# Optimization experiments

Hardware: AMD Instinct MI355X
Metric: run time of the kernel (lower is better)

Reference implementation:

```python
import jax, jax.numpy as jnp
import numpy as np
from jax import lax

B, C, L = 8, 256, 2048
DK, DV, KS = 256, 256, 3
PAD = (KS - 1) // 2  # odd kernel -> dilation 1, same-length padding


def conv1d(x, w, b):
    # x: (B, C, L), w: (O, C, KS), b: (O,)
    y = lax.conv_general_dilated(
        x, w, window_strides=(1,), padding=[(PAD, PAD)],
        rhs_dilation=(1,), dimension_numbers=("NCH", "OIH", "NCH"))
    return y + b[None, :, None]


def setup_inputs() -> dict:
    key = jax.random.key(0)
    ks = jax.random.split(key, 7)
    sc = 1.0 / np.sqrt(C * KS)
    return {
        "x": jax.random.normal(ks[0], (B, C, L), dtype=jnp.float32),
        "Wq": jax.random.normal(ks[1], (DK, C, KS), dtype=jnp.float32) * sc,
        "bq": jnp.zeros((DK,), dtype=jnp.float32),
        "Wk": jax.random.normal(ks[2], (DK, C, KS), dtype=jnp.float32) * sc,
        "bk": jnp.zeros((DK,), dtype=jnp.float32),
        "Wv": jax.random.normal(ks[3], (DV, C, KS), dtype=jnp.float32) * sc,
        "bv": jnp.zeros((DV,), dtype=jnp.float32),
    }


def reference(x, Wq, bq, Wk, bk, Wv, bv):
    Q = conv1d(x, Wq, bq)  # (B, DK, L)
    K = conv1d(x, Wk, bk)  # (B, DK, L)
    V = conv1d(x, Wv, bv)  # (B, DV, L)
    # A = softmax(Q^T K / sqrt(dk)) over key axis
    scores = jnp.einsum("bdq,bdk->bqk", Q, K) / jnp.sqrt(jnp.float32(DK))
    A = jax.nn.softmax(scores, axis=2)  # (B, L, L)
    H = jnp.einsum("bqk,bdk->bdq", A, V)  # (B, DV, L)
    return H
```

## Files before the change

kernel.cpp:

```cpp
#include <hip/hip_runtime.h>
#include <hip/hip_bf16.h>
#include <stdint.h>


typedef __bf16 bf16;
typedef __bf16 bf16x2 __attribute__((ext_vector_type(2)));
typedef __bf16 bf16x4 __attribute__((ext_vector_type(4)));
typedef __bf16 bf16x8 __attribute__((ext_vector_type(8)));
typedef float f32x4 __attribute__((ext_vector_type(4)));
typedef uint32_t u32x4 __attribute__((ext_vector_type(4)));
typedef __attribute__((address_space(1))) const uint32_t cu32_as1;
typedef __attribute__((address_space(3))) uint32_t u32_as3;

#define DEVI __device__ __forceinline__
#define LOG2E 1.44269504088896f

DEVI void async_copy16(const void* g, void* l) {
  __builtin_amdgcn_global_load_lds((cu32_as1*)g, (u32_as3*)l, 16, 0, 0);
}

DEVI void block_sync() {
  asm volatile("" ::: "memory");
  __builtin_amdgcn_sched_barrier(0);
  __builtin_amdgcn_s_barrier();
  __builtin_amdgcn_sched_barrier(0);
  asm volatile("" ::: "memory");
}

#define VMCNT(n) asm volatile("s_waitcnt vmcnt(" #n ")" ::: "memory")

__global__ void prep_wx(const float* __restrict__ Wq, const float* __restrict__ Wk,
                        const float* __restrict__ Wv, const float* __restrict__ bq,
                        const float* __restrict__ bk, const float* __restrict__ bv,
                        bf16* __restrict__ W2, float* __restrict__ biasA,
                        const float* __restrict__ x, bf16* __restrict__ xT) {
  __shared__ float tile[64][33];
  const int blk = blockIdx.x;
  const int t = threadIdx.x;
  if (blk < 2304) {
    const float QSC = 0.0625f * LOG2E;
    int idx = blk * 256 + t;
    if (idx < 768 * 768) {
      int o = idx / 768, kk = idx - o * 768;
      int ks = kk >> 8, c = kk & 255;
      const float* W = (o < 256) ? Wq : ((o < 512) ? Wk : Wv);
      int ol = o & 255;
      float w = W[ol * 768 + c * 3 + ks];
      if (o < 256) w *= QSC;
      W2[o * 768 + kk] = (bf16)w;
    }
    if (idx < 768) {
      float v;
      if (idx < 256) v = bq[idx] * QSC;
      else if (idx < 512) v = bk[idx - 256];
      else v = bv[idx - 512];
      biasA[idx] = v;
    }
    return;
  }
  const int bid = blk - 2304;
  const int b = bid >> 8;
  const int rest = bid & 255;
  const int ct = rest & 3;
  const int lt = rest >> 2;
  const int c0 = ct * 64, l0 = lt * 32;
  const float* xb = x + (size_t)b * 256 * 2048;
#pragma unroll
  for (int i = 0; i < 8; ++i) {
    const int cc = (t >> 5) + i * 8;
    tile[cc][t & 31] = xb[(size_t)(c0 + cc) * 2048 + l0 + (t & 31)];
  }
  __syncthreads();
  bf16* xTb = xT + (size_t)b * 2050 * 256;
#pragma unroll
  for (int j = 0; j < 8; ++j) {
    const int ll = (t >> 6) + j * 4;
    xTb[(size_t)(l0 + ll + 1) * 256 + c0 + (t & 63)] = (bf16)tile[t & 63][ll];
  }
  if (lt == 0 && t < 64) xTb[c0 + t] = (bf16)0.f;
  if (lt == 63 && t < 64) xTb[(size_t)2049 * 256 + c0 + t] = (bf16)0.f;
}

__launch_bounds__(256, 2)
__global__ void conv_gemm(const bf16* __restrict__ W2, const bf16* __restrict__ xT,
                          const float* __restrict__ biasA, bf16* __restrict__ QT,
                          bf16* __restrict__ KT, bf16* __restrict__ V) {
  __shared__ bf16 Alds[128 * 64];
  __shared__ bf16 Blds[128 * 64];
  const int t = threadIdx.x;
  const int w = t >> 6, lane = t & 63;
  const int g = lane >> 4, lr = lane & 15;
  const int wr = w >> 1, wc = w & 1;
  const int bid = blockIdx.x;
  const int b = bid & 7;
  const int rest = bid >> 3;
  const int ot = rest % 6;
  const int lt = rest / 6;
  const int l0 = lt * 128;

  const bf16* xTb = xT + (size_t)b * 2050 * 256;
  const bf16* Ab = W2 + (size_t)(ot * 128) * 768;

  const int srow = t >> 3;
  const int scb = ((t & 7) * 16) ^ ((srow & 7) << 4);

  f32x4 acc[4][4];
#pragma unroll
  for (int i = 0; i < 4; ++i)
#pragma unroll
    for (int j = 0; j < 4; ++j) acc[i][j] = (f32x4){0.f, 0.f, 0.f, 0.f};

  for (int step = 0; step < 12; ++step) {
    const int kk = step * 64;
    const int ks = kk >> 8;
    const int c0 = kk & 255;
    const bf16* As = Ab + kk + (scb >> 1);
    const bf16* Bs = xTb + (size_t)(l0 + ks) * 256 + c0 + (scb >> 1);
#pragma unroll
    for (int i = 0; i < 4; ++i) {
      const int row = srow + i * 32;
      async_copy16(As + (size_t)row * 768, (char*)Alds + w * 1024 + i * 4096);
      async_copy16(Bs + (size_t)row * 256, (char*)Blds + w * 1024 + i * 4096);
    }
    asm volatile("s_waitcnt vmcnt(0)" ::: "memory");
    __syncthreads();
#pragma unroll
    for (int sub = 0; sub < 2; ++sub) {
      bf16x8 af[4], bfr[4];
#pragma unroll
      for (int mf = 0; mf < 4; ++mf) {
        const int row = wr * 64 + mf * 16 + lr;
        const int cb = (sub * 64 + g * 16) ^ ((row & 7) << 4);
        af[mf] = *(const bf16x8*)((const char*)Alds + row * 128 + cb);
      }
#pragma unroll
      for (int nf = 0; nf < 4; ++nf) {
        const int row = wc * 64 + nf * 16 + lr;
        const int cb = (sub * 64 + g * 16) ^ ((row & 7) << 4);
        bfr[nf] = *(const bf16x8*)((const char*)Blds + row * 128 + cb);
      }
#pragma unroll
      for (int mf = 0; mf < 4; ++mf)
#pragma unroll
        for (int nf = 0; nf < 4; ++nf)
          acc[mf][nf] = __builtin_amdgcn_mfma_f32_16x16x32_bf16(af[mf], bfr[nf], acc[mf][nf], 0, 0, 0);
    }
    __syncthreads();
  }

  const int obase = ot * 128 + wr * 64;
  const int lbase = l0 + wc * 64;
  if (ot < 4) {
    bf16* dst = ((ot < 2) ? QT : KT) + (size_t)b * 2048 * 256;
#pragma unroll
    for (int mf = 0; mf < 4; ++mf) {
      const int og = obase + mf * 16 + g * 4;
      float bb[4];
#pragma unroll
      for (int r = 0; r < 4; ++r) bb[r] = biasA[og + r];
#pragma unroll
      for (int nf = 0; nf < 4; ++nf) {
        const int l = lbase + nf * 16 + lr;
        bf16x4 pk;
#pragma unroll
        for (int r = 0; r < 4; ++r) pk[r] = (bf16)(acc[mf][nf][r] + bb[r]);
        *(bf16x4*)(dst + (size_t)l * 256 + (og & 255)) = pk;
      }
    }
  } else {
    bf16* dst = V + (size_t)b * 256 * 2048;
#pragma unroll
    for (int mf = 0; mf < 4; ++mf) {
      const int og = obase + mf * 16 + g * 4;
      float bb[4];
#pragma unroll
      for (int r = 0; r < 4; ++r) bb[r] = biasA[og + r];
      const int ov = og - 512;
#pragma unroll
      for (int nf = 0; nf < 4; ++nf) {
        const int l = lbase + nf * 16 + lr;
#pragma unroll
        for (int r = 0; r < 4; ++r)
          dst[(size_t)(ov + r) * 2048 + l] = (bf16)(acc[mf][nf][r] + bb[r]);
      }
    }
  }
}

__launch_bounds__(256, 2)
__global__ void attn(const bf16* __restrict__ QT, const bf16* __restrict__ KT,
                     const bf16* __restrict__ V, bf16* __restrict__ Opart,
                     float* __restrict__ Sl) {
  __shared__ bf16 Klds[2 * 32 * 256];
  __shared__ bf16 Vlds[128 * 64];
  const int t = threadIdx.x;
  const int w = t >> 6, lane = t & 63;
  const int g = lane >> 4, lr = lane & 15;
  const int bid = blockIdx.x;
  const int b = bid & 7;
  const int kvh = (bid >> 3) & 3;
  const int qt = bid >> 5;
  const int q0w = qt * 128 + w * 32;
  const int kb0 = kvh * 512;
  const bf16* QTb = QT + (size_t)b * 2048 * 256;
  const bf16* KTb = KT + (size_t)b * 2048 * 256;
  const bf16* Vb = V + (size_t)b * 256 * 2048;

  auto stageK = [&](int kt, int p) {
#pragma unroll
    for (int i = 0; i < 4; ++i) {
      const int row = i * 8 + (t >> 5);
      const int col = ((t & 31) ^ row) * 8;
      const bf16* src = KTb + (size_t)(kb0 + kt * 32 + row) * 256 + col;
      async_copy16(src, (char*)Klds + p * 16384 + i * 4096 + t * 16);
    }
  };
  auto stageV = [&](int kt) {
#pragma unroll
    for (int i = 0; i < 4; ++i) {
      const int row = i * 32 + (t >> 3);
      const int ls = (t & 7) ^ (row & 7);
      const int d = row * 2 + (ls >> 2);
      const int k0 = (ls & 3) * 8;
      const bf16* src = Vb + (size_t)d * 2048 + kb0 + kt * 32 + k0;
      async_copy16(src, (char*)Vlds + i * 4096 + t * 16);
    }
  };

  bf16x8 qreg[2][8];
#pragma unroll
  for (int qfr = 0; qfr < 2; ++qfr)
#pragma unroll
    for (int ds = 0; ds < 8; ++ds)
      qreg[qfr][ds] = *(const bf16x8*)(QTb + (size_t)(q0w + qfr * 16 + lr) * 256 + ds * 32 + g * 8);

  f32x4 oacc[16][2];
#pragma unroll
  for (int i = 0; i < 16; ++i) {
    oacc[i][0] = (f32x4){0.f, 0.f, 0.f, 0.f};
    oacc[i][1] = (f32x4){0.f, 0.f, 0.f, 0.f};
  }
  float l_acc[2] = {0.f, 0.f};

  stageV(0);
  stageK(0, 0);
  stageK(1, 1);

  for (int kt = 0; kt < 16; ++kt) {
    const int p = kt & 1;
    if (kt == 15) { VMCNT(0); } else { VMCNT(4); }
    block_sync();

    f32x4 sT[2][2];
#pragma unroll
    for (int kfr = 0; kfr < 2; ++kfr)
#pragma unroll
      for (int qfr = 0; qfr < 2; ++qfr) sT[kfr][qfr] = (f32x4){0.f, 0.f, 0.f, 0.f};
    __builtin_amdgcn_s_setprio(1);
#pragma unroll
    for (int ds = 0; ds < 8; ++ds) {
      bf16x8 kf[2];
#pragma unroll
      for (int kfr = 0; kfr < 2; ++kfr) {
        const int row = kfr * 16 + lr;
        kf[kfr] = *(const bf16x8*)((const char*)Klds + p * 16384 + row * 512 +
                                   (((ds * 4 + g) ^ row) * 16));
      }
#pragma unroll
      for (int kfr = 0; kfr < 2; ++kfr)
#pragma unroll
        for (int qfr = 0; qfr < 2; ++qfr)
          sT[kfr][qfr] = __builtin_amdgcn_mfma_f32_16x16x32_bf16(kf[kfr], qreg[qfr][ds], sT[kfr][qfr], 0, 0, 0);
    }
    __builtin_amdgcn_s_setprio(0);

#pragma unroll
    for (int kfr = 0; kfr < 2; ++kfr)
#pragma unroll
      for (int qfr = 0; qfr < 2; ++qfr)
#pragma unroll
        for (int r = 0; r < 4; ++r) {
          float pe = __builtin_exp2f(sT[kfr][qfr][r]);
          sT[kfr][qfr][r] = pe;
          l_acc[qfr] += pe;
        }

    bf16x8 pB[2];
#pragma unroll
    for (int qfr = 0; qfr < 2; ++qfr) {
      uint32_t wq[2][2];
#pragma unroll
      for (int kfr = 0; kfr < 2; ++kfr)
#pragma unroll
        for (int pp = 0; pp < 2; ++pp) {
          bf16x2 pr;
          pr[0] = (bf16)sT[kfr][qfr][2 * pp];
          pr[1] = (bf16)sT[kfr][qfr][2 * pp + 1];
          wq[kfr][pp] = __builtin_bit_cast(uint32_t, pr);
        }
      uint32_t bw[4];
#pragma unroll
      for (int j = 0; j < 4; ++j) {
        const int srcLane = ((g & 1) * 2 + (j >> 1)) * 16 + lr;
        const uint32_t a = (uint32_t)__shfl((int)wq[0][j & 1], srcLane, 64);
        const uint32_t bb = (uint32_t)__shfl((int)wq[1][j & 1], srcLane, 64);
        bw[j] = (lane < 32) ? a : bb;
      }
      u32x4 v4 = {bw[0], bw[1], bw[2], bw[3]};
      pB[qfr] = __builtin_bit_cast(bf16x8, v4);
    }

    __builtin_amdgcn_s_setprio(1);
#pragma unroll
    for (int dfr = 0; dfr < 16; ++dfr) {
      const int row = dfr * 8 + (lr >> 1);
      bf16x8 vf = *(const bf16x8*)((const char*)Vlds + row * 128 +
                                   ((((lr & 1) * 4 + g) ^ ((lr >> 1) & 7)) * 16));
      oacc[dfr][0] = __builtin_amdgcn_mfma_f32_16x16x32_bf16(vf, pB[0], oacc[dfr][0], 0, 0, 0);
      oacc[dfr][1] = __builtin_amdgcn_mfma_f32_16x16x32_bf16(vf, pB[1], oacc[dfr][1], 0, 0, 0);
    }
    __builtin_amdgcn_s_setprio(0);
    block_sync();
    if (kt < 15) stageV(kt + 1);
    if (kt < 14) stageK(kt + 2, p);
  }

#pragma unroll
  for (int qfr = 0; qfr < 2; ++qfr) {
    float rv = l_acc[qfr];
    rv += __shfl_xor(rv, 16, 64);
    rv += __shfl_xor(rv, 32, 64);
    l_acc[qfr] = rv;
  }

  bf16* Op = Opart + (size_t)bid * 128 * 256;
#pragma unroll
  for (int qfr = 0; qfr < 2; ++qfr) {
    const int ql = w * 32 + qfr * 16 + lr;
#pragma unroll
    for (int dfr = 0; dfr < 16; ++dfr) {
      const int d0 = dfr * 16 + g * 4;
      bf16x4 pk;
#pragma unroll
      for (int r = 0; r < 4; ++r) pk[r] = (bf16)oacc[dfr][qfr][r];
      *(bf16x4*)(Op + (size_t)ql * 256 + d0) = pk;
    }
    if (g == 0) Sl[bid * 128 + ql] = l_acc[qfr];
  }
}

__launch_bounds__(256)
__global__ void merge_p(const bf16* __restrict__ Opart, const float* __restrict__ Sl,
                        float* __restrict__ H) {
  __shared__ float Ocomb[32][257];
  const int bid = blockIdx.x;
  const int b = bid & 7;
  const int qt = (bid >> 3) & 15;
  const int qc = bid >> 7;
  const int t = threadIdx.x;
  const int g2 = t >> 5, lane2 = t & 31;
  float* Hb = H + (size_t)b * 256 * 2048 + qt * 128 + qc * 32;

#pragma unroll
  for (int qb = 0; qb < 4; ++qb) {
    const int qq = qb * 8 + g2;
    const int ql = qc * 32 + qq;
    float wsum = 0.f;
    float o[8];
#pragma unroll
    for (int j = 0; j < 8; ++j) o[j] = 0.f;
#pragma unroll
    for (int kvh = 0; kvh < 4; ++kvh) {
      const int blk = b + 8 * kvh + 32 * qt;
      wsum += Sl[blk * 128 + ql];
      bf16x8 v = *(const bf16x8*)(Opart + ((size_t)blk * 128 + ql) * 256 + lane2 * 8);
#pragma unroll
      for (int j = 0; j < 8; ++j) o[j] += (float)v[j];
    }
    const float inv = 1.f / wsum;
#pragma unroll
    for (int j = 0; j < 8; ++j) Ocomb[qq][lane2 * 8 + j] = o[j] * inv;
  }
  __syncthreads();
  const int q = t & 31;
  const int dbase = (t >> 5) * 32;
#pragma unroll
  for (int j = 0; j < 32; ++j) {
    const int d = dbase + j;
    Hb[(size_t)d * 2048 + q] = Ocomb[q][d];
  }
}

extern "C" void kernel_launch(void* const* d_in, const int* in_sizes, int n_in,
                              void* d_out, int out_size, void* d_ws, size_t ws_size,
                              hipStream_t stream) {
  (void)in_sizes; (void)n_in; (void)out_size; (void)ws_size;
  const float* x = (const float*)d_in[0];
  const float* Wq = (const float*)d_in[1];
  const float* bq = (const float*)d_in[2];
  const float* Wk = (const float*)d_in[3];
  const float* bk = (const float*)d_in[4];
  const float* Wv = (const float*)d_in[5];
  const float* bv = (const float*)d_in[6];
  char* ws = (char*)d_ws;
  bf16* xT = (bf16*)(ws + 0);
  bf16* W2 = (bf16*)(ws + 8396800);
  float* biasA = (float*)(ws + 9576448);
  bf16* QT = (bf16*)(ws + 9580544);
  bf16* KT = (bf16*)(ws + 17969152);
  bf16* V = (bf16*)(ws + 26357760);
  bf16* Opart = (bf16*)(ws + 34746368);
  float* Sl = (float*)(ws + 68300800);
  float* H = (float*)d_out;

  prep_wx<<<dim3(4352), dim3(256), 0, stream>>>(Wq, Wk, Wv, bq, bk, bv, W2, biasA, x, xT);
  conv_gemm<<<dim3(768), dim3(256), 0, stream>>>(W2, xT, biasA, QT, KT, V);
  attn<<<dim3(512), dim3(256), 0, stream>>>(QT, KT, V, Opart, Sl);
  merge_p<<<dim3(512), dim3(256), 0, stream>>>(Opart, Sl, H);
}
```

Before: 106.1 us.

## Use 64-key tiles with split K/V staging and 16x16x16 MFMA for PV

The attention kernel now processes 64 keys per iteration instead of 32 and drops the double-buffered K tile. K for the next tile is prefetched right after the QK^T MFMAs, and V after the PV MFMAs. The PV product switches to the 16x16x16 bf16 MFMA so the exponentiated scores can feed the B operand directly from the QK accumulator layout, removing the cross-lane shuffle repack. The trade-off is twice as many narrower MFMAs for PV, extra barriers per iteration, and K loads that are less overlapped without double buffering.

```diff
diff --git a/kernel.cpp b/kernel.cpp
--- a/kernel.cpp
+++ b/kernel.cpp
@@ -4,11 +4,10 @@
 
 
 typedef __bf16 bf16;
-typedef __bf16 bf16x2 __attribute__((ext_vector_type(2)));
 typedef __bf16 bf16x4 __attribute__((ext_vector_type(4)));
 typedef __bf16 bf16x8 __attribute__((ext_vector_type(8)));
+typedef short s16x4 __attribute__((ext_vector_type(4)));
 typedef float f32x4 __attribute__((ext_vector_type(4)));
-typedef uint32_t u32x4 __attribute__((ext_vector_type(4)));
 typedef __attribute__((address_space(1))) const uint32_t cu32_as1;
 typedef __attribute__((address_space(3))) uint32_t u32_as3;
 
@@ -191,8 +190,8 @@
 __global__ void attn(const bf16* __restrict__ QT, const bf16* __restrict__ KT,
                      const bf16* __restrict__ V, bf16* __restrict__ Opart,
                      float* __restrict__ Sl) {
-  __shared__ bf16 Klds[2 * 32 * 256];
-  __shared__ bf16 Vlds[128 * 64];
+  __shared__ bf16 Klds[64 * 256];
+  __shared__ bf16 Vlds[256 * 64];
   const int t = threadIdx.x;
   const int w = t >> 6, lane = t & 63;
   const int g = lane >> 4, lr = lane & 15;
@@ -206,23 +205,21 @@
   const bf16* KTb = KT + (size_t)b * 2048 * 256;
   const bf16* Vb = V + (size_t)b * 256 * 2048;
 
-  auto stageK = [&](int kt, int p) {
-#pragma unroll
-    for (int i = 0; i < 4; ++i) {
+  auto stageK = [&](int kt) {
+#pragma unroll
+    for (int i = 0; i < 8; ++i) {
       const int row = i * 8 + (t >> 5);
-      const int col = ((t & 31) ^ row) * 8;
-      const bf16* src = KTb + (size_t)(kb0 + kt * 32 + row) * 256 + col;
-      async_copy16(src, (char*)Klds + p * 16384 + i * 4096 + t * 16);
+      const int col = ((t & 31) ^ (row & 31)) * 8;
+      const bf16* src = KTb + (size_t)(kb0 + kt * 64 + row) * 256 + col;
+      async_copy16(src, (char*)Klds + i * 4096 + t * 16);
     }
   };
   auto stageV = [&](int kt) {
 #pragma unroll
-    for (int i = 0; i < 4; ++i) {
+    for (int i = 0; i < 8; ++i) {
       const int row = i * 32 + (t >> 3);
-      const int ls = (t & 7) ^ (row & 7);
-      const int d = row * 2 + (ls >> 2);
-      const int k0 = (ls & 3) * 8;
-      const bf16* src = Vb + (size_t)d * 2048 + kb0 + kt * 32 + k0;
+      const int koff = ((t & 7) ^ (row & 7)) * 8;
+      const bf16* src = Vb + (size_t)row * 2048 + kb0 + kt * 64 + koff;
       async_copy16(src, (char*)Vlds + i * 4096 + t * 16);
     }
   };
@@ -242,87 +239,71 @@
   }
   float l_acc[2] = {0.f, 0.f};
 
+  stageK(0);
   stageV(0);
-  stageK(0, 0);
-  stageK(1, 1);
-
-  for (int kt = 0; kt < 16; ++kt) {
-    const int p = kt & 1;
-    if (kt == 15) { VMCNT(0); } else { VMCNT(4); }
+
+  for (int kt = 0; kt < 8; ++kt) {
+    VMCNT(8);
     block_sync();
 
-    f32x4 sT[2][2];
-#pragma unroll
-    for (int kfr = 0; kfr < 2; ++kfr)
+    f32x4 sT[4][2];
+#pragma unroll
+    for (int kfr = 0; kfr < 4; ++kfr)
 #pragma unroll
       for (int qfr = 0; qfr < 2; ++qfr) sT[kfr][qfr] = (f32x4){0.f, 0.f, 0.f, 0.f};
     __builtin_amdgcn_s_setprio(1);
 #pragma unroll
     for (int ds = 0; ds < 8; ++ds) {
-      bf16x8 kf[2];
-#pragma unroll
-      for (int kfr = 0; kfr < 2; ++kfr) {
+      bf16x8 kf[4];
+#pragma unroll
+      for (int kfr = 0; kfr < 4; ++kfr) {
         const int row = kfr * 16 + lr;
-        kf[kfr] = *(const bf16x8*)((const char*)Klds + p * 16384 + row * 512 +
-                                   (((ds * 4 + g) ^ row) * 16));
-      }
-#pragma unroll
-      for (int kfr = 0; kfr < 2; ++kfr)
+        kf[kfr] = *(const bf16x8*)((const char*)Klds + row * 512 +
+                                   (((ds * 4 + g) ^ (row & 31)) * 16));
+      }
+#pragma unroll
+      for (int kfr = 0; kfr < 4; ++kfr)
 #pragma unroll
         for (int qfr = 0; qfr < 2; ++qfr)
           sT[kfr][qfr] = __builtin_amdgcn_mfma_f32_16x16x32_bf16(kf[kfr], qreg[qfr][ds], sT[kfr][qfr], 0, 0, 0);
     }
     __builtin_amdgcn_s_setprio(0);
-
-#pragma unroll
-    for (int kfr = 0; kfr < 2; ++kfr)
-#pragma unroll
-      for (int qfr = 0; qfr < 2; ++qfr)
+    block_sync();
+    if (kt < 7) stageK(kt + 1);
+
+    s16x4 pB16[4][2];
+#pragma unroll
+    for (int kfr = 0; kfr < 4; ++kfr)
+#pragma unroll
+      for (int qfr = 0; qfr < 2; ++qfr) {
+        bf16x4 pk;
 #pragma unroll
         for (int r = 0; r < 4; ++r) {
           float pe = __builtin_exp2f(sT[kfr][qfr][r]);
-          sT[kfr][qfr][r] = pe;
           l_acc[qfr] += pe;
+          pk[r] = (bf16)pe;
         }
-
-    bf16x8 pB[2];
-#pragma unroll
-    for (int qfr = 0; qfr < 2; ++qfr) {
-      uint32_t wq[2][2];
-#pragma unroll
-      for (int kfr = 0; kfr < 2; ++kfr)
-#pragma unroll
-        for (int pp = 0; pp < 2; ++pp) {
-          bf16x2 pr;
-          pr[0] = (bf16)sT[kfr][qfr][2 * pp];
-          pr[1] = (bf16)sT[kfr][qfr][2 * pp + 1];
-          wq[kfr][pp] = __builtin_bit_cast(uint32_t, pr);
-        }
-      uint32_t bw[4];
-#pragma unroll
-      for (int j = 0; j < 4; ++j) {
-        const int srcLane = ((g & 1) * 2 + (j >> 1)) * 16 + lr;
-        const uint32_t a = (uint32_t)__shfl((int)wq[0][j & 1], srcLane, 64);
-        const uint32_t bb = (uint32_t)__shfl((int)wq[1][j & 1], srcLane, 64);
-        bw[j] = (lane < 32) ? a : bb;
-      }
-      u32x4 v4 = {bw[0], bw[1], bw[2], bw[3]};
-      pB[qfr] = __builtin_bit_cast(bf16x8, v4);
-    }
+        pB16[kfr][qfr] = __builtin_bit_cast(s16x4, pk);
+      }
+
+    VMCNT(8);
+    block_sync();
 
     __builtin_amdgcn_s_setprio(1);
 #pragma unroll
     for (int dfr = 0; dfr < 16; ++dfr) {
-      const int row = dfr * 8 + (lr >> 1);
-      bf16x8 vf = *(const bf16x8*)((const char*)Vlds + row * 128 +
-                                   ((((lr & 1) * 4 + g) ^ ((lr >> 1) & 7)) * 16));
-      oacc[dfr][0] = __builtin_amdgcn_mfma_f32_16x16x32_bf16(vf, pB[0], oacc[dfr][0], 0, 0, 0);
-      oacc[dfr][1] = __builtin_amdgcn_mfma_f32_16x16x32_bf16(vf, pB[1], oacc[dfr][1], 0, 0, 0);
+      const int row = dfr * 16 + lr;
+#pragma unroll
+      for (int kfr = 0; kfr < 4; ++kfr) {
+        const int slot = (kfr * 2 + (g >> 1)) ^ (row & 7);
+        s16x4 vf = *(const s16x4*)((const char*)Vlds + row * 128 + slot * 16 + (g & 1) * 8);
+        oacc[dfr][0] = __builtin_amdgcn_mfma_f32_16x16x16bf16_1k(vf, pB16[kfr][0], oacc[dfr][0], 0, 0, 0);
+        oacc[dfr][1] = __builtin_amdgcn_mfma_f32_16x16x16bf16_1k(vf, pB16[kfr][1], oacc[dfr][1], 0, 0, 0);
+      }
     }
     __builtin_amdgcn_s_setprio(0);
     block_sync();
-    if (kt < 15) stageV(kt + 1);
-    if (kt < 14) stageK(kt + 2, p);
+    if (kt < 7) stageV(kt + 1);
   }
 
 #pragma unroll
```

New measurement: 179.1 us. 1.69x slower.
